# Kernel optimization log

Hardware: AMD Instinct MI355X
Metric: run time of the kernel (lower is better)

The kernel has to match this reference:

```python
import jax, jax.numpy as jnp
import numpy as np

EPS = 1e-6
ROPE_THETA = 10000.0


def rmsnorm(x, w):
    return x * jax.lax.rsqrt(jnp.mean(x * x, axis=-1, keepdims=True) + EPS) * w


def rope(q, k, seq_len, head_dim):
    # rotate-half RoPE. q,k: [b, h, s, d]
    half = head_dim // 2
    inv_freq = 1.0 / (ROPE_THETA ** (jnp.arange(0, half, dtype=jnp.float32) / half))
    t = jnp.arange(seq_len, dtype=jnp.float32)
    freqs = jnp.outer(t, inv_freq)                      # [s, d/2]
    cos = jnp.concatenate([jnp.cos(freqs)] * 2, axis=-1)  # [s, d]
    sin = jnp.concatenate([jnp.sin(freqs)] * 2, axis=-1)

    def rot(x):
        x1, x2 = x[..., :half], x[..., half:]
        return jnp.concatenate([-x2, x1], axis=-1)

    return q * cos + rot(q) * sin, k * cos + rot(k) * sin


def setup_inputs() -> dict:
    key = jax.random.key(0)
    ks = jax.random.split(key, 8)
    B, S, D, E, F = 4, 2048, 1024, 8, 4096
    sd = 0.02
    return {
        "x": jax.random.normal(ks[0], (B, S, D), dtype=jnp.float32),
        "mapped_tokens": jax.random.randint(ks[1], (B, S), 0, E, dtype=jnp.int32),
        "rms1_w": jnp.ones((D,), dtype=jnp.float32),
        "wqkv": jax.random.normal(ks[2], (D, 3 * D), dtype=jnp.float32) * sd,
        "wo": jax.random.normal(ks[3], (D, D), dtype=jnp.float32) * sd,
        "rms2_w": jnp.ones((D,), dtype=jnp.float32),
        "w1": jax.random.normal(ks[4], (E, D, F), dtype=jnp.float32) * sd,
        "w2": jax.random.normal(ks[5], (E, F, D), dtype=jnp.float32) * sd,
    }


def attention(x, wqkv, wo, num_heads=16):
    B, S, D = x.shape
    hd = D // num_heads
    qkv = x @ wqkv                                       # [b, s, 3D]
    q, k, v = jnp.split(qkv, 3, axis=-1)
    def heads(t):
        return t.reshape(B, S, num_heads, hd).transpose(0, 2, 1, 3)  # [b,h,s,d]
    q, k, v = heads(q), heads(k), heads(v)
    q, k = rope(q, k, S, hd)
    scores = jnp.einsum("bhqd,bhkd->bhqk", q, k) / jnp.sqrt(jnp.float32(hd))
    causal = jnp.tril(jnp.ones((S, S), dtype=bool))
    scores = jnp.where(causal, scores, jnp.finfo(scores.dtype).min)
    attn = jax.nn.softmax(scores, axis=-1)
    out = jnp.einsum("bhqk,bhkd->bhqd", attn, v)
    out = out.transpose(0, 2, 1, 3).reshape(B, S, D)
    return out @ wo


def moe_hash_ffn(x, mapped_tokens, w1, w2):
    # hash-routed MoE: each token goes to exactly one expert given by mapped_tokens
    B, S, D = x.shape
    E = w1.shape[0]
    xf = x.reshape(B * S, D)
    mt = mapped_tokens.reshape(B * S)
    out = jnp.zeros_like(xf)
    for e in range(E):  # small fixed expert count
        y = jax.nn.gelu(xf @ w1[e]) @ w2[e]
        out = out + jnp.where((mt == e)[:, None], y, 0.0)
    return out.reshape(B, S, D)


def reference(x, mapped_tokens, rms1_w, wqkv, wo, rms2_w, w1, w2):
    h = x + attention(rmsnorm(x, rms1_w), wqkv, wo)
    out = h + moe_hash_ffn(rmsnorm(h, rms2_w), mapped_tokens, w1, w2)
    return out
```

## Files before the change

kernel.cpp:

```cpp
#include <hip/hip_runtime.h>
#include <hip/hip_bf16.h>
#include <stdint.h>

typedef __hip_bfloat16 bf16;
typedef __attribute__((ext_vector_type(8))) short bf16x8;
typedef __attribute__((ext_vector_type(4))) float f32x4;
typedef __attribute__((ext_vector_type(16))) float f32x16;
typedef unsigned int u32;

static constexpr int Bsz = 4, S = 2048, D = 1024, E = 8, F = 4096, NH = 16, HD = 64;
static constexpr int TOK = Bsz * S;
static constexpr int SLOTS = TOK + E * 128;

#define DEV __device__ __forceinline__

DEV void async16(const bf16* g, bf16* l) {
  __builtin_amdgcn_global_load_lds((const __attribute__((address_space(1))) u32*)g,
                                   (__attribute__((address_space(3))) u32*)l, 16, 0, 0);
}

DEV u32 lds_off(const bf16* p) {
  return (u32)(uintptr_t)(__attribute__((address_space(3))) bf16*)p;
}

DEV bf16x8 dsr128(u32 addr) {
  bf16x8 d;
  asm volatile("ds_read_b128 %0, %1" : "=v"(d) : "v"(addr));
  return d;
}

DEV float gelu_fast(float x) {
  const float z = 0.7978845608028654f * (x + 0.044715f * x * x * x);
  return x / (1.f + __expf(-2.f * z));
}

DEV u32 cvtpk(float lo, float hi) {
  u32 r;
  asm("v_cvt_pk_bf16_f32 %0, %1, %2" : "=v"(r) : "v"(lo), "v"(hi));
  return r;
}


__global__ void cvt_transpose(const float* __restrict__ in, bf16* __restrict__ out, int R, int C) {
  __shared__ float t[64][65];
  const size_t zoff = (size_t)blockIdx.z * R * C;
  const int c0 = blockIdx.x * 64, r0 = blockIdx.y * 64;
  const int tid = threadIdx.x;
  const int lrow = tid >> 4, lcol = (tid & 15) * 4;
#pragma unroll
  for (int p = 0; p < 4; ++p) {
    const int r = lrow + p * 16;
    const float4 v = *(const float4*)(in + zoff + (size_t)(r0 + r) * C + c0 + lcol);
    t[r][lcol] = v.x; t[r][lcol + 1] = v.y; t[r][lcol + 2] = v.z; t[r][lcol + 3] = v.w;
  }
  __syncthreads();
  const int ow = tid >> 3, je = (tid & 7) * 8;
#pragma unroll
  for (int p = 0; p < 2; ++p) {
    const int oc = ow + p * 32;
    union { bf16x8 v; bf16 b[8]; } o8;
#pragma unroll
    for (int j = 0; j < 8; ++j) o8.b[j] = __float2bfloat16(t[je + j][oc]);
    *(bf16x8*)(out + zoff + (size_t)(c0 + oc) * R + r0 + je) = o8.v;
  }
}

__global__ void rope_tables(float* __restrict__ cosT, float* __restrict__ sinT) {
  const int s = blockIdx.x * 2 + (threadIdx.x >> 5);
  const int i = threadIdx.x & 31;
  const float inv_freq = powf(10000.f, -(float)i / 32.f);
  const float ang = (float)s * inv_freq;
  cosT[s * 32 + i] = cosf(ang);
  sinT[s * 32 + i] = sinf(ang);
}

__global__ void rmsnorm_k(const float* __restrict__ x, const float* __restrict__ w, bf16* __restrict__ out) {
  const size_t row = blockIdx.x;
  const int tid = threadIdx.x;
  const float4 v = *(const float4*)(x + row * D + tid * 4);
  float ss = v.x * v.x + v.y * v.y + v.z * v.z + v.w * v.w;
#pragma unroll
  for (int off = 1; off < 64; off <<= 1) ss += __shfl_xor(ss, off);
  __shared__ float red[4];
  if ((tid & 63) == 0) red[tid >> 6] = ss;
  __syncthreads();
  const float inv = rsqrtf((red[0] + red[1] + red[2] + red[3]) * (1.f / D) + 1e-6f);
  const float4 wv = *(const float4*)(w + tid * 4);
  union { ushort4 u; bf16 b[4]; } o;
  o.b[0] = __float2bfloat16(v.x * inv * wv.x);
  o.b[1] = __float2bfloat16(v.y * inv * wv.y);
  o.b[2] = __float2bfloat16(v.z * inv * wv.z);
  o.b[3] = __float2bfloat16(v.w * inv * wv.w);
  *(ushort4*)((unsigned short*)out + row * D + tid * 4) = o.u;
}

__global__ void route_init(int* counts, int* cursors, int* perm) {
  const int i = blockIdx.x * 256 + threadIdx.x;
  if (i < E) { counts[i] = 0; cursors[i] = 0; }
  if (i < SLOTS) perm[i] = -1;
}
__global__ void route_count(const int* __restrict__ mt, int* counts) {
  const int i = blockIdx.x * 256 + threadIdx.x;
  if (i < TOK) atomicAdd(&counts[mt[i]], 1);
}
__global__ void route_offsets(const int* __restrict__ counts, int* aoff) {
  if (threadIdx.x == 0) {
    int off = 0; aoff[0] = 0;
    for (int e = 0; e < E; ++e) { off += (counts[e] + 127) & ~127; aoff[e + 1] = off; }
  }
}
__global__ void route_scatter(const int* __restrict__ mt, const int* __restrict__ aoff,
                              int* cursors, int* perm) {
  const int i = blockIdx.x * 256 + threadIdx.x;
  if (i < TOK) { const int e = mt[i]; perm[aoff[e] + atomicAdd(&cursors[e], 1)] = i; }
}

__global__ __launch_bounds__(512) void qkv8p(
    const bf16* __restrict__ A, const bf16* __restrict__ Bt,
    const float* __restrict__ c_t, const float* __restrict__ s_t,
    bf16* __restrict__ o_q, bf16* __restrict__ o_k, bf16* __restrict__ o_v) {
  constexpr int K = 1024, NT = K / 64;
  __shared__ __align__(16) bf16 LA[2][256 * 64];
  __shared__ __align__(16) bf16 LB[2][256 * 64];
  const int tid = threadIdx.x;
  const int lane = tid & 63, wv = tid >> 6;
  const int wm = wv >> 2, wn = wv & 3;
  const int rl = lane & 15, kg = lane >> 4;
  const int gx = gridDim.x;
  const int nwg = gx * gridDim.y;
  int bid = blockIdx.y * gx + blockIdx.x;
  bid = (bid & 7) * (nwg >> 3) + (bid >> 3);
  const int nbase = (bid % gx) * 256, mbase = (bid / gx) * 256;
  f32x4 acc[8][4] = {};
  const int srow = tid >> 3;
  const int sc = (tid & 7) ^ ((srow >> 1) & 7);
  const bf16* Ag = A + (size_t)(mbase + srow) * K + sc * 8;
  const bf16* Bg = Bt + (size_t)(nbase + srow) * K + sc * 8;

  auto stage = [&](int t, int h) {
    const int buf = t & 1;
    const int mat = h >> 1, rh = h & 1;
    const bf16* src = (mat ? Bg : Ag) + (size_t)(rh * 128) * K + t * 64;
    bf16* dst = (mat ? &LB[buf][0] : &LA[buf][0]) + rh * 128 * 64 + tid * 8;
    async16(src, dst);
    async16(src + (size_t)64 * K, dst + 64 * 64);
  };

  bf16x8 bfr[4];
  auto phaseC = [&](int t, int ks, int mih, bool loadB) {
    const int buf = t & 1;
    const u32 ab = lds_off(&LA[buf][0]);
    const u32 bb = lds_off(&LB[buf][0]);
    bf16x8 af[4];
#pragma unroll
    for (int mi = 0; mi < 4; ++mi) {
      const int row = wm * 128 + mih * 64 + mi * 16 + rl;
      const u32 ph = (u32)((ks * 4 + kg) ^ ((row >> 1) & 7));
      af[mi] = dsr128(ab + (u32)row * 128 + ph * 16);
    }
    if (loadB) {
#pragma unroll
      for (int ni = 0; ni < 4; ++ni) {
        const int row = wn * 64 + ni * 16 + rl;
        const u32 ph = (u32)((ks * 4 + kg) ^ ((row >> 1) & 7));
        bfr[ni] = dsr128(bb + (u32)row * 128 + ph * 16);
      }
    }
    asm volatile("s_waitcnt lgkmcnt(0)" ::: "memory");
    __builtin_amdgcn_sched_barrier(0);
    __builtin_amdgcn_s_setprio(1);
#pragma unroll
    for (int mi = 0; mi < 4; ++mi)
#pragma unroll
      for (int ni = 0; ni < 4; ++ni)
        acc[mih * 4 + mi][ni] =
            __builtin_amdgcn_mfma_f32_16x16x32_bf16(af[mi], bfr[ni], acc[mih * 4 + mi][ni], 0, 0, 0);
    __builtin_amdgcn_s_setprio(0);
  };

  stage(0, 0); stage(0, 1); stage(0, 2); stage(0, 3);
  for (int t = 0; t < NT; ++t) {
    const bool more = (t + 1 < NT);
#pragma unroll
    for (int p = 0; p < 4; ++p) {
      if (p == 0) {
        if (more) {
          stage(t + 1, 0);
          asm volatile("s_waitcnt vmcnt(2)" ::: "memory");
        } else {
          asm volatile("s_waitcnt vmcnt(0)" ::: "memory");
        }
        __builtin_amdgcn_s_barrier();
        __builtin_amdgcn_sched_barrier(0);
      } else if (more) {
        stage(t + 1, p);
      }
      phaseC(t, p >> 1, p & 1, (p & 1) == 0);
      __builtin_amdgcn_s_barrier();
      __builtin_amdgcn_sched_barrier(0);
    }
  }

  const int colbase = nbase + wn * 64;
  const int part = colbase >> 10;
  const int head = (colbase & 1023) >> 6;
  const float qs = (part == 0) ? 0.18033688011112042f : 1.f;
#pragma unroll
  for (int ai = 0; ai < 8; ++ai) {
    const int rowoff = (ai >> 2) * 64 + (ai & 3) * 16;
#pragma unroll
    for (int r = 0; r < 4; ++r) {
      const int grow = mbase + wm * 128 + rowoff + kg * 4 + r;
      const int bb = grow >> 11, sp = grow & (S - 1);
      if (part == 2) {
#pragma unroll
        for (int ni = 0; ni < 4; ++ni) {
          const int d = ni * 16 + rl;
          o_v[((size_t)(bb * NH + head) * HD + d) * S + sp] = __float2bfloat16(acc[ai][ni][r]);
        }
      } else {
        bf16* dst = (part == 0) ? o_q : o_k;
        const size_t base = ((size_t)(bb * NH + head) * S + sp) * HD;
#pragma unroll
        for (int np = 0; np < 2; ++np) {
          const int i = np * 16 + rl;
          const float c = c_t[sp * 32 + i];
          const float sn = s_t[sp * 32 + i];
          const float lo = acc[ai][np][r];
          const float hi = acc[ai][np + 2][r];
          dst[base + i] = __float2bfloat16((lo * c - hi * sn) * qs);
          dst[base + i + 32] = __float2bfloat16((hi * c + lo * sn) * qs);
        }
      }
    }
  }
}

template <int EPI, int BM>
__global__ __launch_bounds__(2 * BM, 4) void gemm_bt(
    const bf16* __restrict__ A, const bf16* __restrict__ Bt, int M, int N, int K,
    const int* __restrict__ aoff, long long estride,
    const float* __restrict__ xres, float* __restrict__ o_h,
    bf16* __restrict__ o_act,
    const int* __restrict__ perm, const float* __restrict__ hres, float* __restrict__ o_out) {
  constexpr int WN = BM / 64;
  constexpr int MR = BM / 2;
  constexpr int M_FR = MR / 16;
  __shared__ __align__(16) bf16 As[2][BM * 32];
  __shared__ __align__(16) bf16 Bs[2][BM * 32];
  const int tid = threadIdx.x;
  const int lane = tid & 63, wv = tid >> 6;
  const int wm = wv / WN, wn = wv % WN;
  const int rl = lane & 15, kg = lane >> 4;
  const int gx = gridDim.x;
  const int nwg = gx * gridDim.y;
  int bid = blockIdx.y * gx + blockIdx.x;
  bid = (bid & 7) * (nwg >> 3) + (bid >> 3);
  const int nbase = (bid % gx) * BM, mbase = (bid / gx) * BM;
  const bf16* Btp = Bt;
  if constexpr (EPI >= 2) {
    if (mbase >= aoff[E]) return;
    int e = 0;
#pragma unroll
    for (int t = 0; t < E - 1; ++t) e += (mbase >= aoff[t + 1]) ? 1 : 0;
    Btp = Bt + (size_t)e * estride;
  }
  f32x4 acc[M_FR][4] = {};
  const int srow = tid >> 2;
  const int sc = (tid & 3) ^ ((srow >> 1) & 3);
  const bf16* Agp[2];
#pragma unroll
  for (int c = 0; c < 2; ++c) {
    int rowslot = mbase + c * MR + srow;
    if constexpr (EPI == 2) {
      const int t = perm[rowslot];
      rowslot = (t < 0) ? 0 : t;
    }
    Agp[c] = A + (size_t)rowslot * K + sc * 8;
  }
  const bf16* Bg = Btp + (size_t)(nbase + srow) * K + sc * 8;

  auto stage = [&](int bi, int ko) {
#pragma unroll
    for (int c = 0; c < 2; ++c) {
      async16(Agp[c] + ko, &As[bi][c * MR * 32 + wv * 512]);
      async16(Bg + (size_t)(c * MR) * K + ko, &Bs[bi][c * MR * 32 + wv * 512]);
    }
  };
  auto compute = [&](int bi) {
    bf16x8 af[M_FR], bfr[4];
#pragma unroll
    for (int mi = 0; mi < M_FR; ++mi) {
      const int row = wm * MR + mi * 16 + rl;
      af[mi] = *(const bf16x8*)&As[bi][row * 32 + ((kg ^ ((row >> 1) & 3))) * 8];
    }
#pragma unroll
    for (int ni = 0; ni < 4; ++ni) {
      const int row = wn * 64 + ni * 16 + rl;
      bfr[ni] = *(const bf16x8*)&Bs[bi][row * 32 + ((kg ^ ((row >> 1) & 3))) * 8];
    }
#pragma unroll
    for (int mi = 0; mi < M_FR; ++mi)
#pragma unroll
      for (int ni = 0; ni < 4; ++ni)
        acc[mi][ni] = __builtin_amdgcn_mfma_f32_16x16x32_bf16(af[mi], bfr[ni], acc[mi][ni], 0, 0, 0);
  };

  const int nk = K >> 5;
  stage(0, 0);
  __syncthreads();
  for (int kb = 0; kb < nk; ++kb) {
    if (kb + 1 < nk) stage((kb + 1) & 1, (kb + 1) * 32);
    compute(kb & 1);
    __syncthreads();
  }

#pragma unroll
  for (int mi = 0; mi < M_FR; ++mi) {
#pragma unroll
    for (int ni = 0; ni < 4; ++ni) {
#pragma unroll
      for (int r = 0; r < 4; ++r) {
        const int grow = mbase + wm * MR + mi * 16 + kg * 4 + r;
        const int gcol = nbase + wn * 64 + ni * 16 + rl;
        const float vv = acc[mi][ni][r];
        if constexpr (EPI == 1) {
          const size_t ix = (size_t)grow * 1024 + gcol;
          o_h[ix] = xres[ix] + vv;
        } else if constexpr (EPI == 2) {
          o_act[(size_t)grow * 4096 + gcol] = __float2bfloat16(gelu_fast(vv));
        } else {
          const int t = perm[grow];
          if (t >= 0) {
            const size_t ix = (size_t)t * 1024 + gcol;
            o_out[ix] = hres[ix] + vv;
          }
        }
      }
    }
  }
}

__global__ __launch_bounds__(256, 3) void attn_kernel(const bf16* __restrict__ Qb,
                                                      const bf16* __restrict__ Kb,
                                                      const bf16* __restrict__ Vt,
                                                      bf16* __restrict__ AO) {
  __shared__ __align__(16) bf16 Kl[2][64 * 64];
  __shared__ __align__(16) bf16 Vl[2][64 * 64];
  const int bh = blockIdx.x;
  const int tid = threadIdx.x;
  const int w = tid >> 6, lane = tid & 63;
  const int q = lane & 31, hi = lane >> 5;
  const bf16* Qp = Qb + (size_t)bh * S * HD;
  const bf16* Kp = Kb + (size_t)bh * S * HD;
  const bf16* Vp = Vt + (size_t)bh * S * HD;
  const int b = bh >> 4, h = bh & 15;
  const int qblk = (S / 128 - 1) - blockIdx.y;
  const int qrow0 = qblk * 128 + w * 32;
  const int ntb = qblk * 2 + 2;
  const int ntw = (qrow0 >> 6) + 1;
  const int srow = tid >> 3;
  const int schk = tid & 7;

  bf16x8 qf[4];
#pragma unroll
  for (int t = 0; t < 4; ++t)
    qf[t] = *(const bf16x8*)(Qp + (size_t)(qrow0 + q) * HD + t * 16 + hi * 8);
  f32x16 oa0 = {}, oa1 = {};
  float m = -INFINITY, l = 0.f;

  auto stageKV = [&](int buf, int kvb) {
#pragma unroll
    for (int hh = 0; hh < 2; ++hh) {
      const int row = srow + hh * 32;
      const int c = schk ^ (row & 7);
      async16(Kp + (size_t)(kvb + row) * HD + c * 8, &Kl[buf][tid * 8 + hh * 2048]);
      async16(Vp + (size_t)row * S + kvb + c * 8, &Vl[buf][tid * 8 + hh * 2048]);
    }
  };
  auto packP = [&](float s0, float s1, float s2, float s3,
                   float s4, float s5, float s6, float s7) -> bf16x8 {
    u32 x0 = cvtpk(s0, s1), x1 = cvtpk(s2, s3);
    u32 y0 = cvtpk(s4, s5), y1 = cvtpk(s6, s7);
    asm volatile("v_permlane32_swap_b32 %0, %1" : "+v"(x0), "+v"(y0));
    asm volatile("v_permlane32_swap_b32 %0, %1" : "+v"(x1), "+v"(y1));
    union { u32 w[4]; bf16x8 v; } u;
    u.w[0] = x0; u.w[1] = x1; u.w[2] = y0; u.w[3] = y1;
    return u.v;
  };

  stageKV(0, 0);
  __syncthreads();
  for (int kt = 0; kt < ntb; ++kt) {
    const int buf = kt & 1;
    const int kvb = kt * 64;
    if (kt + 1 < ntb) stageKV(buf ^ 1, kvb + 64);
    if (kt < ntw) {
      f32x16 sa0 = {}, sa1 = {};
#pragma unroll
      for (int t = 0; t < 4; ++t) {
        const int c = (2 * t + hi) ^ (q & 7);
        const bf16x8 kf0 = *(const bf16x8*)&Kl[buf][q * 64 + c * 8];
        sa0 = __builtin_amdgcn_mfma_f32_32x32x16_bf16(kf0, qf[t], sa0, 0, 0, 0);
      }
#pragma unroll
      for (int t = 0; t < 4; ++t) {
        const int c = (2 * t + hi) ^ (q & 7);
        const bf16x8 kf1 = *(const bf16x8*)&Kl[buf][(q + 32) * 64 + c * 8];
        sa1 = __builtin_amdgcn_mfma_f32_32x32x16_bf16(kf1, qf[t], sa1, 0, 0, 0);
      }
      if (kvb + 63 > qrow0) {
#pragma unroll
        for (int r = 0; r < 16; ++r) {
          const int kloc = (r & 3) + 8 * (r >> 2) + 4 * hi;
          sa0[r] = (kvb + kloc > qrow0 + q) ? -3.0e38f : sa0[r];
          sa1[r] = (kvb + 32 + kloc > qrow0 + q) ? -3.0e38f : sa1[r];
        }
      }
      float vm;
      {
        float a0 = fmaxf(fmaxf(sa0[0], sa0[1]), fmaxf(sa0[2], sa0[3]));
        float a1 = fmaxf(fmaxf(sa0[4], sa0[5]), fmaxf(sa0[6], sa0[7]));
        float a2 = fmaxf(fmaxf(sa0[8], sa0[9]), fmaxf(sa0[10], sa0[11]));
        float a3 = fmaxf(fmaxf(sa0[12], sa0[13]), fmaxf(sa0[14], sa0[15]));
        float b0 = fmaxf(fmaxf(sa1[0], sa1[1]), fmaxf(sa1[2], sa1[3]));
        float b1 = fmaxf(fmaxf(sa1[4], sa1[5]), fmaxf(sa1[6], sa1[7]));
        float b2 = fmaxf(fmaxf(sa1[8], sa1[9]), fmaxf(sa1[10], sa1[11]));
        float b3 = fmaxf(fmaxf(sa1[12], sa1[13]), fmaxf(sa1[14], sa1[15]));
        vm = fmaxf(fmaxf(fmaxf(a0, a1), fmaxf(a2, a3)), fmaxf(fmaxf(b0, b1), fmaxf(b2, b3)));
      }
      vm = fmaxf(vm, __shfl_xor(vm, 32));
      const bool grow = __any(vm > m);
      const float mn = grow ? fmaxf(m, vm) : m;
#pragma unroll
      for (int r = 0; r < 16; ++r) {
        sa0[r] = exp2f(sa0[r] - mn);
        sa1[r] = exp2f(sa1[r] - mn);
      }
      float ps;
      {
        float a0 = (sa0[0] + sa0[1]) + (sa0[2] + sa0[3]);
        float a1 = (sa0[4] + sa0[5]) + (sa0[6] + sa0[7]);
        float a2 = (sa0[8] + sa0[9]) + (sa0[10] + sa0[11]);
        float a3 = (sa0[12] + sa0[13]) + (sa0[14] + sa0[15]);
        float b0 = (sa1[0] + sa1[1]) + (sa1[2] + sa1[3]);
        float b1 = (sa1[4] + sa1[5]) + (sa1[6] + sa1[7]);
        float b2 = (sa1[8] + sa1[9]) + (sa1[10] + sa1[11]);
        float b3 = (sa1[12] + sa1[13]) + (sa1[14] + sa1[15]);
        ps = ((a0 + a1) + (a2 + a3)) + ((b0 + b1) + (b2 + b3));
      }
      ps += __shfl_xor(ps, 32);
      if (grow) {
        const float scs = exp2f(m - mn);
        l = l * scs + ps;
        m = mn;
#pragma unroll
        for (int r = 0; r < 16; ++r) { oa0[r] *= scs; oa1[r] *= scs; }
      } else {
        l += ps;
      }
      {
        auto vrd = [&](int r, int s2i) -> bf16x8 {
          const int c = (2 * s2i + hi) ^ (r & 7);
          return *(const bf16x8*)&Vl[buf][r * 64 + c * 8];
        };
        const bf16x8 pf0 = packP(sa0[0], sa0[1], sa0[2], sa0[3], sa0[4], sa0[5], sa0[6], sa0[7]);
        oa0 = __builtin_amdgcn_mfma_f32_32x32x16_bf16(vrd(q, 0), pf0, oa0, 0, 0, 0);
        oa1 = __builtin_amdgcn_mfma_f32_32x32x16_bf16(vrd(q + 32, 0), pf0, oa1, 0, 0, 0);
        const bf16x8 pf1 = packP(sa0[8], sa0[9], sa0[10], sa0[11], sa0[12], sa0[13], sa0[14], sa0[15]);
        oa0 = __builtin_amdgcn_mfma_f32_32x32x16_bf16(vrd(q, 1), pf1, oa0, 0, 0, 0);
        oa1 = __builtin_amdgcn_mfma_f32_32x32x16_bf16(vrd(q + 32, 1), pf1, oa1, 0, 0, 0);
        const bf16x8 pf2 = packP(sa1[0], sa1[1], sa1[2], sa1[3], sa1[4], sa1[5], sa1[6], sa1[7]);
        oa0 = __builtin_amdgcn_mfma_f32_32x32x16_bf16(vrd(q, 2), pf2, oa0, 0, 0, 0);
        oa1 = __builtin_amdgcn_mfma_f32_32x32x16_bf16(vrd(q + 32, 2), pf2, oa1, 0, 0, 0);
        const bf16x8 pf3 = packP(sa1[8], sa1[9], sa1[10], sa1[11], sa1[12], sa1[13], sa1[14], sa1[15]);
        oa0 = __builtin_amdgcn_mfma_f32_32x32x16_bf16(vrd(q, 3), pf3, oa0, 0, 0, 0);
        oa1 = __builtin_amdgcn_mfma_f32_32x32x16_bf16(vrd(q + 32, 3), pf3, oa1, 0, 0, 0);
      }
    }
    __syncthreads();
  }
  const float invl = 1.f / l;
#pragma unroll
  for (int n = 0; n < 2; ++n) {
#pragma unroll
    for (int g = 0; g < 4; ++g) {
      union { ushort4 u4; bf16 bb[4]; } o4;
#pragma unroll
      for (int mi = 0; mi < 4; ++mi) {
        const float val = (n ? oa1[4 * g + mi] : oa0[4 * g + mi]) * invl;
        o4.bb[mi] = __float2bfloat16(val);
      }
      const int d = n * 32 + 8 * g + 4 * hi;
      *(ushort4*)&AO[((size_t)(b * S + qrow0 + q)) * D + h * HD + d] = o4.u4;
    }
  }
}

extern "C" void kernel_launch(void* const* d_in, const int* in_sizes, int n_in,
                              void* d_out, int out_size, void* d_ws, size_t ws_size,
                              hipStream_t stream) {
  const float* x = (const float*)d_in[0];
  const int* mt = (const int*)d_in[1];
  const float* rms1 = (const float*)d_in[2];
  const float* wqkv = (const float*)d_in[3];
  const float* wo = (const float*)d_in[4];
  const float* rms2 = (const float*)d_in[5];
  const float* w1 = (const float*)d_in[6];
  const float* w2 = (const float*)d_in[7];
  float* out = (float*)d_out;
  (void)in_sizes; (void)n_in; (void)out_size; (void)ws_size;

  char* ws = (char*)d_ws;
  size_t off = 0;
  auto alloc = [&](size_t b) { void* p = ws + off; off = (off + b + 255) & ~(size_t)255; return p; };
  bf16* wqkvT = (bf16*)alloc((size_t)3072 * 1024 * 2);
  bf16* woT   = (bf16*)alloc((size_t)1024 * 1024 * 2);
  bf16* w1T   = (bf16*)alloc((size_t)E * F * D * 2);
  bf16* w2T   = (bf16*)alloc((size_t)E * D * F * 2);
  float* cosT = (float*)alloc((size_t)S * 32 * 4);
  float* sinT = (float*)alloc((size_t)S * 32 * 4);
  float* hbuf = (float*)alloc((size_t)TOK * D * 4);
  bf16* xn2   = (bf16*)alloc((size_t)TOK * D * 2);
  int* counts  = (int*)alloc(E * 4);
  int* cursors = (int*)alloc(E * 4);
  int* aoff    = (int*)alloc((E + 1) * 4);
  int* perm    = (int*)alloc(SLOTS * 4);
  char* R = (char*)alloc((size_t)5 * TOK * D * 2);
  bf16* xn = (bf16*)R;
  bf16* qb = (bf16*)(R + (size_t)1 * TOK * D * 2);
  bf16* kb = (bf16*)(R + (size_t)2 * TOK * D * 2);
  bf16* vb = (bf16*)(R + (size_t)3 * TOK * D * 2);
  bf16* ao = (bf16*)(R + (size_t)4 * TOK * D * 2);
  bf16* act = (bf16*)R;

  cvt_transpose<<<dim3(3072 / 64, 1024 / 64, 1), 256, 0, stream>>>(wqkv, wqkvT, 1024, 3072);
  cvt_transpose<<<dim3(1024 / 64, 1024 / 64, 1), 256, 0, stream>>>(wo, woT, 1024, 1024);
  cvt_transpose<<<dim3(4096 / 64, 1024 / 64, E), 256, 0, stream>>>(w1, w1T, 1024, 4096);
  cvt_transpose<<<dim3(1024 / 64, 4096 / 64, E), 256, 0, stream>>>(w2, w2T, 4096, 1024);
  rope_tables<<<dim3(S / 2), 64, 0, stream>>>(cosT, sinT);
  route_init<<<dim3((SLOTS + 255) / 256), 256, 0, stream>>>(counts, cursors, perm);
  route_count<<<dim3(TOK / 256), 256, 0, stream>>>(mt, counts);
  route_offsets<<<dim3(1), 64, 0, stream>>>(counts, aoff);
  route_scatter<<<dim3(TOK / 256), 256, 0, stream>>>(mt, aoff, cursors, perm);
  rmsnorm_k<<<dim3(TOK), 256, 0, stream>>>(x, rms1, xn);
  qkv8p<<<dim3(3072 / 256, TOK / 256), 512, 0, stream>>>(
      xn, wqkvT, cosT, sinT, qb, kb, vb);
  attn_kernel<<<dim3(64, S / 128), 256, 0, stream>>>(qb, kb, vb, ao);
  gemm_bt<1, 128><<<dim3(1024 / 128, TOK / 128), 256, 0, stream>>>(
      ao, woT, TOK, 1024, 1024, nullptr, 0, x, hbuf, nullptr, nullptr, nullptr, nullptr);
  rmsnorm_k<<<dim3(TOK), 256, 0, stream>>>(hbuf, rms2, xn2);
  gemm_bt<2, 128><<<dim3(4096 / 128, SLOTS / 128), 256, 0, stream>>>(
      xn2, w1T, SLOTS, 4096, 1024, aoff, (long long)F * D, nullptr, nullptr, act, perm,
      nullptr, nullptr);
  gemm_bt<3, 128><<<dim3(1024 / 128, SLOTS / 128), 256, 0, stream>>>(
      act, w2T, SLOTS, 1024, 4096, aoff, (long long)D * F, nullptr, nullptr, nullptr, perm,
      hbuf, out);
}
```

Measured before the change: 627.7 us.

## Use 256-row tiled 512-thread GEMM kernel for MoE FFN layers

Adds a dedicated ffn2p kernel for the two expert GEMMs, using 256-row M tiles with 512 threads (256x256 for FFN1, 256x128 for FFN2). Expert padding moves from 128 to 256 slots so each tile stays within one expert. gemm_bt is trimmed to the attention output projection only. Larger tiles raise operand reuse per LDS stage, but padding waste and per-thread register pressure go up and occupancy may drop.

Measured after the change: 692.6 us. +10.3%, slower.

```diff
diff --git a/kernel.cpp b/kernel.cpp
--- a/kernel.cpp
+++ b/kernel.cpp
@@ -10,7 +10,7 @@
 
 static constexpr int Bsz = 4, S = 2048, D = 1024, E = 8, F = 4096, NH = 16, HD = 64;
 static constexpr int TOK = Bsz * S;
-static constexpr int SLOTS = TOK + E * 128;
+static constexpr int SLOTS = TOK + E * 256;
 
 #define DEV __device__ __forceinline__
 
@@ -106,7 +106,7 @@
 __global__ void route_offsets(const int* __restrict__ counts, int* aoff) {
   if (threadIdx.x == 0) {
     int off = 0; aoff[0] = 0;
-    for (int e = 0; e < E; ++e) { off += (counts[e] + 127) & ~127; aoff[e + 1] = off; }
+    for (int e = 0; e < E; ++e) { off += (counts[e] + 255) & ~255; aoff[e + 1] = off; }
   }
 }
 __global__ void route_scatter(const int* __restrict__ mt, const int* __restrict__ aoff,
@@ -236,13 +236,110 @@
   }
 }
 
+template <int EPI, int BN>
+__global__ __launch_bounds__(512) void ffn2p(
+    const bf16* __restrict__ A, const bf16* __restrict__ Bt,
+    const int* __restrict__ aoff, long long estride,
+    bf16* __restrict__ o_act,
+    const int* __restrict__ perm, const float* __restrict__ hres,
+    float* __restrict__ o_out) {
+  constexpr int K = (EPI == 2) ? 1024 : 4096;
+  constexpr int BM = 256;
+  constexpr int WNW = BN / 64;
+  constexpr int MW = BM / (8 / WNW);
+  constexpr int M_FR = MW / 16;
+  __shared__ __align__(16) bf16 As[2][BM * 32];
+  __shared__ __align__(16) bf16 Bs[2][BN * 32];
+  const int tid = threadIdx.x;
+  const int lane = tid & 63, wv = tid >> 6;
+  const int wm = wv / WNW, wn = wv % WNW;
+  const int rl = lane & 15, kg = lane >> 4;
+  const int gx = gridDim.x;
+  const int nwg = gx * gridDim.y;
+  int bid = blockIdx.y * gx + blockIdx.x;
+  bid = (bid & 7) * (nwg >> 3) + (bid >> 3);
+  const int nbase = (bid % gx) * BN, mbase = (bid / gx) * BM;
+  if (mbase >= aoff[E]) return;
+  int e = 0;
+#pragma unroll
+  for (int t = 0; t < E - 1; ++t) e += (mbase >= aoff[t + 1]) ? 1 : 0;
+  const bf16* Btp = Bt + (size_t)e * estride;
+
+  f32x4 acc[M_FR][4] = {};
+  const int srow = tid >> 2;
+  const int sc = (tid & 3) ^ ((srow >> 1) & 3);
+  const bf16* Agp[2];
+#pragma unroll
+  for (int c = 0; c < 2; ++c) {
+    int slot = mbase + c * 128 + srow;
+    if constexpr (EPI == 2) { const int pt = perm[slot]; slot = (pt < 0) ? 0 : pt; }
+    Agp[c] = A + (size_t)slot * K + sc * 8;
+  }
+  const bf16* Bg = Btp + (size_t)(nbase + srow) * K + sc * 8;
+
+  auto stage = [&](int bi, int ko) {
+#pragma unroll
+    for (int c = 0; c < 2; ++c)
+      async16(Agp[c] + ko, &As[bi][c * 128 * 32 + tid * 8]);
+#pragma unroll
+    for (int c = 0; c < BN / 128; ++c)
+      async16(Bg + (size_t)(c * 128) * K + ko, &Bs[bi][c * 128 * 32 + tid * 8]);
+  };
+  auto compute = [&](int bi) {
+    bf16x8 af[M_FR], bfr[4];
+#pragma unroll
+    for (int mi = 0; mi < M_FR; ++mi) {
+      const int row = wm * MW + mi * 16 + rl;
+      af[mi] = *(const bf16x8*)&As[bi][row * 32 + ((kg ^ ((row >> 1) & 3))) * 8];
+    }
+#pragma unroll
+    for (int ni = 0; ni < 4; ++ni) {
+      const int row = wn * 64 + ni * 16 + rl;
+      bfr[ni] = *(const bf16x8*)&Bs[bi][row * 32 + ((kg ^ ((row >> 1) & 3))) * 8];
+    }
+#pragma unroll
+    for (int mi = 0; mi < M_FR; ++mi)
+#pragma unroll
+      for (int ni = 0; ni < 4; ++ni)
+        acc[mi][ni] = __builtin_amdgcn_mfma_f32_16x16x32_bf16(af[mi], bfr[ni], acc[mi][ni], 0, 0, 0);
+  };
+
+  const int nk = K >> 5;
+  stage(0, 0);
+  __syncthreads();
+  for (int kb = 0; kb < nk; ++kb) {
+    if (kb + 1 < nk) stage((kb + 1) & 1, (kb + 1) * 32);
+    compute(kb & 1);
+    __syncthreads();
+  }
+
+#pragma unroll
+  for (int mi = 0; mi < M_FR; ++mi) {
+#pragma unroll
+    for (int ni = 0; ni < 4; ++ni) {
+#pragma unroll
+      for (int r = 0; r < 4; ++r) {
+        const int grow = mbase + wm * MW + mi * 16 + kg * 4 + r;
+        const int gcol = nbase + wn * 64 + ni * 16 + rl;
+        const float vv = acc[mi][ni][r];
+        if constexpr (EPI == 2) {
+          o_act[(size_t)grow * 4096 + gcol] = __float2bfloat16(gelu_fast(vv));
+        } else {
+          const int tk = perm[grow];
+          if (tk >= 0) {
+            const size_t ix = (size_t)tk * 1024 + gcol;
+            o_out[ix] = hres[ix] + vv;
+          }
+        }
+      }
+    }
+  }
+}
+
 template <int EPI, int BM>
 __global__ __launch_bounds__(2 * BM, 4) void gemm_bt(
     const bf16* __restrict__ A, const bf16* __restrict__ Bt, int M, int N, int K,
-    const int* __restrict__ aoff, long long estride,
-    const float* __restrict__ xres, float* __restrict__ o_h,
-    bf16* __restrict__ o_act,
-    const int* __restrict__ perm, const float* __restrict__ hres, float* __restrict__ o_out) {
+    const float* __restrict__ xres, float* __restrict__ o_h) {
   constexpr int WN = BM / 64;
   constexpr int MR = BM / 2;
   constexpr int M_FR = MR / 16;
@@ -257,28 +354,13 @@
   int bid = blockIdx.y * gx + blockIdx.x;
   bid = (bid & 7) * (nwg >> 3) + (bid >> 3);
   const int nbase = (bid % gx) * BM, mbase = (bid / gx) * BM;
-  const bf16* Btp = Bt;
-  if constexpr (EPI >= 2) {
-    if (mbase >= aoff[E]) return;
-    int e = 0;
-#pragma unroll
-    for (int t = 0; t < E - 1; ++t) e += (mbase >= aoff[t + 1]) ? 1 : 0;
-    Btp = Bt + (size_t)e * estride;
-  }
   f32x4 acc[M_FR][4] = {};
   const int srow = tid >> 2;
   const int sc = (tid & 3) ^ ((srow >> 1) & 3);
   const bf16* Agp[2];
 #pragma unroll
-  for (int c = 0; c < 2; ++c) {
-    int rowslot = mbase + c * MR + srow;
-    if constexpr (EPI == 2) {
-      const int t = perm[rowslot];
-      rowslot = (t < 0) ? 0 : t;
-    }
-    Agp[c] = A + (size_t)rowslot * K + sc * 8;
-  }
-  const bf16* Bg = Btp + (size_t)(nbase + srow) * K + sc * 8;
+  for (int c = 0; c < 2; ++c) Agp[c] = A + (size_t)(mbase + c * MR + srow) * K + sc * 8;
+  const bf16* Bg = Bt + (size_t)(nbase + srow) * K + sc * 8;
 
   auto stage = [&](int bi, int ko) {
 #pragma unroll
@@ -323,19 +405,8 @@
       for (int r = 0; r < 4; ++r) {
         const int grow = mbase + wm * MR + mi * 16 + kg * 4 + r;
         const int gcol = nbase + wn * 64 + ni * 16 + rl;
-        const float vv = acc[mi][ni][r];
-        if constexpr (EPI == 1) {
-          const size_t ix = (size_t)grow * 1024 + gcol;
-          o_h[ix] = xres[ix] + vv;
-        } else if constexpr (EPI == 2) {
-          o_act[(size_t)grow * 4096 + gcol] = __float2bfloat16(gelu_fast(vv));
-        } else {
-          const int t = perm[grow];
-          if (t >= 0) {
-            const size_t ix = (size_t)t * 1024 + gcol;
-            o_out[ix] = hres[ix] + vv;
-          }
-        }
+        const size_t ix = (size_t)grow * 1024 + gcol;
+        o_h[ix] = xres[ix] + acc[mi][ni][r];
       }
     }
   }
@@ -548,12 +619,10 @@
       xn, wqkvT, cosT, sinT, qb, kb, vb);
   attn_kernel<<<dim3(64, S / 128), 256, 0, stream>>>(qb, kb, vb, ao);
   gemm_bt<1, 128><<<dim3(1024 / 128, TOK / 128), 256, 0, stream>>>(
-      ao, woT, TOK, 1024, 1024, nullptr, 0, x, hbuf, nullptr, nullptr, nullptr, nullptr);
+      ao, woT, TOK, 1024, 1024, x, hbuf);
   rmsnorm_k<<<dim3(TOK), 256, 0, stream>>>(hbuf, rms2, xn2);
-  gemm_bt<2, 128><<<dim3(4096 / 128, SLOTS / 128), 256, 0, stream>>>(
-      xn2, w1T, SLOTS, 4096, 1024, aoff, (long long)F * D, nullptr, nullptr, act, perm,
-      nullptr, nullptr);
-  gemm_bt<3, 128><<<dim3(1024 / 128, SLOTS / 128), 256, 0, stream>>>(
-      act, w2T, SLOTS, 1024, 4096, aoff, (long long)D * F, nullptr, nullptr, nullptr, perm,
-      hbuf, out);
-}
+  ffn2p<2, 256><<<dim3(4096 / 256, SLOTS / 256), 512, 0, stream>>>(
+      xn2, w1T, aoff, (long long)F * D, act, perm, nullptr, nullptr);
+  ffn2p<3, 128><<<dim3(1024 / 128, SLOTS / 256), 512, 0, stream>>>(
+      act, w2T, aoff, (long long)D * F, nullptr, perm, hbuf, out);
+}
```
